# Performance work log

Measured on AMD Instinct MI355X. Metric: run time of the kernel, lower is better.

The kernel has to match this reference:

```python
import jax, jax.numpy as jnp
import numpy as np

EPS = 1e-7  # tf.keras.backend.epsilon()
ROUTINGS = 3


def setup_inputs() -> dict:
    key = jax.random.key(0)
    k1, k2 = jax.random.split(key)
    x = jax.random.normal(k1, (64, 2048, 8), dtype=jnp.float32)
    W = jax.random.normal(k2, (32, 2048, 16, 8), dtype=jnp.float32) * 0.05
    return {"x": x, "W": W}


def _squash(s):
    # source squash: vectors / sqrt(sum(v^2) + eps)
    ssq = jnp.sum(s * s, axis=-1, keepdims=True)
    return s / jnp.sqrt(ssq + EPS)


def reference(x, W):
    # x: [B, N, I]; W: [J, N, D, I]
    # prediction vectors u_hat: [B, J, N, D]
    u_hat = jnp.einsum('bni,jndi->bjnd', x, W)
    b = jnp.zeros(u_hat.shape[:-1], dtype=u_hat.dtype)  # [B, J, N]
    v = None
    for i in range(ROUTINGS):
        c = jax.nn.softmax(b, axis=1)                       # coupling over output caps J
        s = jnp.einsum('bjnd,bjn->bjd', u_hat, c)           # weighted sum over input caps N
        v = _squash(s)                                      # [B, J, D]
        if i < ROUTINGS - 1:
            b = b + jnp.einsum('bjnd,bjd->bjn', u_hat, v)   # agreement update
    return v
```

## Files before the change

### kernel.cpp

```cpp
#include <hip/hip_runtime.h>


#define BB_ 64
#define NN_ 2048
#define II_ 8
#define JJ_ 32
#define DD_ 16
#define NCHUNKS 128
#define CHUNK 16
#define BG 16
#define NBG (BB_ / BG)
#define EPS_ 1e-7f

#define PARTIAL_FLOATS (NCHUNKS * BB_ * JJ_ * DD_)

template <int CTRL>
__device__ __forceinline__ float dpp_add(float v) {
  const int s = __builtin_amdgcn_update_dpp(
      0, __builtin_bit_cast(int, v), CTRL, 0xf, 0xf, true);
  return v + __builtin_bit_cast(float, s);
}
#define DPP_QP_XOR1 0xB1
#define DPP_QP_XOR2 0x4E
#define DPP_HALF_MIRROR 0x141
#define DPP_ROR8 0x128

template <int PHASE>
__global__ __launch_bounds__(256, 2) void caps_phase(
    const float* __restrict__ x, const float* __restrict__ W,
    const float* __restrict__ V, float* __restrict__ partial) {
  const int tid = threadIdx.x;
  const int j = tid >> 3;
  const int p = tid & 7;
  const int chunk = blockIdx.x & (NCHUNKS - 1);
  const int bg = blockIdx.x >> 7;
  const int b0 = bg * BG;
  const int n0 = chunk * CHUNK;

  __shared__ float lmat[BG][JJ_];
  __shared__ float cmat[BG][JJ_];

  float v0r[BG], v1r[BG];
  if (PHASE > 0) {
#pragma unroll
    for (int b = 0; b < BG; ++b) {
      const float2 vv =
          *(const float2*)&V[((size_t)(b0 + b) * JJ_ + j) * DD_ + 2 * p];
      v0r[b] = vv.x;
      v1r[b] = vv.y;
    }
  }

  float s0[BG], s1[BG];
#pragma unroll
  for (int b = 0; b < BG; ++b) {
    s0[b] = 0.f;
    s1[b] = 0.f;
  }

  const float* wp = W + (size_t)j * (NN_ * DD_ * II_) + (size_t)n0 * (DD_ * II_) +
                    (size_t)p * 16;
  float4 wc0 = ((const float4*)wp)[0];
  float4 wc1 = ((const float4*)wp)[1];
  float4 wc2 = ((const float4*)wp)[2];
  float4 wc3 = ((const float4*)wp)[3];

  for (int nl = 0; nl < CHUNK; ++nl) {
    const int n = n0 + nl;
    const int nn = (nl + 1 < CHUNK) ? nl + 1 : nl;
    const float4* np_ = (const float4*)(wp + (size_t)nn * (DD_ * II_));
    const float4 wn0 = np_[0], wn1 = np_[1], wn2 = np_[2], wn3 = np_[3];

    float u0[BG], u1[BG];
#pragma unroll
    for (int b = 0; b < BG; ++b) {
      const float4* __restrict__ xr =
          (const float4*)(x + ((size_t)(b0 + b) * NN_ + n) * II_);
      const float4 xa = xr[0];
      const float4 xb = xr[1];
      u0[b] = wc0.x * xa.x + wc0.y * xa.y + wc0.z * xa.z + wc0.w * xa.w +
              wc1.x * xb.x + wc1.y * xb.y + wc1.z * xb.z + wc1.w * xb.w;
      u1[b] = wc2.x * xa.x + wc2.y * xa.y + wc2.z * xa.z + wc2.w * xa.w +
              wc3.x * xb.x + wc3.y * xb.y + wc3.z * xb.z + wc3.w * xb.w;
    }

    if (PHASE == 0) {
#pragma unroll
      for (int b = 0; b < BG; ++b) {
        s0[b] += u0[b];
        s1[b] += u1[b];
      }
    } else {
#pragma unroll
      for (int b = 0; b < BG; ++b) {
        float lp = u0[b] * v0r[b] + u1[b] * v1r[b];
        lp = dpp_add<DPP_QP_XOR1>(lp);
        lp = dpp_add<DPP_QP_XOR2>(lp);
        lp = dpp_add<DPP_HALF_MIRROR>(lp);
        if (p == 0) lmat[b][j] = lp;
      }
      __syncthreads();
      {
        const int jj = tid & 31;
        const int bb = tid >> 5;
        float e0 = __expf(lmat[bb][jj]);
        float e1 = __expf(lmat[bb + 8][jj]);
        float m0 = e0, m1 = e1;
        m0 = dpp_add<DPP_QP_XOR1>(m0);
        m1 = dpp_add<DPP_QP_XOR1>(m1);
        m0 = dpp_add<DPP_QP_XOR2>(m0);
        m1 = dpp_add<DPP_QP_XOR2>(m1);
        m0 = dpp_add<DPP_HALF_MIRROR>(m0);
        m1 = dpp_add<DPP_HALF_MIRROR>(m1);
        m0 = dpp_add<DPP_ROR8>(m0);
        m1 = dpp_add<DPP_ROR8>(m1);
        m0 += __shfl_xor(m0, 16);
        m1 += __shfl_xor(m1, 16);
        cmat[bb][jj] = e0 * __builtin_amdgcn_rcpf(m0);
        cmat[bb + 8][jj] = e1 * __builtin_amdgcn_rcpf(m1);
      }
      __syncthreads();
#pragma unroll
      for (int b = 0; b < BG; ++b) {
        const float c = cmat[b][j];
        s0[b] += c * u0[b];
        s1[b] += c * u1[b];
      }
    }

    wc0 = wn0;
    wc1 = wn1;
    wc2 = wn2;
    wc3 = wn3;
  }

  const float scale = (PHASE == 0) ? (1.0f / 32.0f) : 1.0f;
#pragma unroll
  for (int b = 0; b < BG; ++b) {
    const size_t off =
        ((size_t)chunk * BB_ + (b0 + b)) * (JJ_ * DD_) + j * DD_ + 2 * p;
    *(float2*)&partial[off] = make_float2(s0[b] * scale, s1[b] * scale);
  }
}

template <int MODE>
__global__ __launch_bounds__(256) void caps_reduce(
    const float* __restrict__ partial, float* __restrict__ V,
    float* __restrict__ out) {
  const int t = blockIdx.x * 256 + threadIdx.x;
  float s = 0.f;
#pragma unroll 8
  for (int c = 0; c < NCHUNKS; ++c)
    s += partial[(size_t)c * (BB_ * JJ_ * DD_) + t];
  float ss = s * s;
  ss += __shfl_xor(ss, 1);
  ss += __shfl_xor(ss, 2);
  ss += __shfl_xor(ss, 4);
  ss += __shfl_xor(ss, 8);
  const float v = s / sqrtf(ss + EPS_);
  if (MODE == 0)
    V[t] = v;
  else if (MODE == 1)
    V[t] += v;
  else
    out[t] = v;
}

extern "C" void kernel_launch(void* const* d_in, const int* in_sizes, int n_in,
                              void* d_out, int out_size, void* d_ws,
                              size_t ws_size, hipStream_t stream) {
  const float* x = (const float*)d_in[0];
  const float* W = (const float*)d_in[1];
  float* out = (float*)d_out;
  float* partial = (float*)d_ws;
  float* V = partial + PARTIAL_FLOATS;

  const dim3 kgrid(NBG * NCHUNKS);
  const dim3 rgrid((BB_ * JJ_ * DD_) / 256);

  caps_phase<0><<<kgrid, 256, 0, stream>>>(x, W, nullptr, partial);
  caps_reduce<0><<<rgrid, 256, 0, stream>>>(partial, V, out);
  caps_phase<1><<<kgrid, 256, 0, stream>>>(x, W, V, partial);
  caps_reduce<1><<<rgrid, 256, 0, stream>>>(partial, V, out);
  caps_phase<2><<<kgrid, 256, 0, stream>>>(x, W, V, partial);
  caps_reduce<2><<<rgrid, 256, 0, stream>>>(partial, V, out);
}
```

Baseline: 214.0 us.

## Halve batch group, raise occupancy, and use packed float2 FMAs

Cuts the per-block batch group from 16 to 8, which doubles the block count and raises the launch-bound occupancy target from 2 to 4 blocks per CU. The prediction dot products become float2 vector math, so the compiler can emit packed FP32 FMAs. The per-iteration softmax now handles one row per thread instead of two. The reduce kernels switch to 128-thread blocks. In exchange, each W chunk is read by twice as many blocks, which increases W traffic unless the cache absorbs it.

```diff
diff --git a/kernel.cpp b/kernel.cpp
--- a/kernel.cpp
+++ b/kernel.cpp
@@ -8,11 +8,13 @@
 #define DD_ 16
 #define NCHUNKS 128
 #define CHUNK 16
-#define BG 16
+#define BG 8
 #define NBG (BB_ / BG)
 #define EPS_ 1e-7f
 
 #define PARTIAL_FLOATS (NCHUNKS * BB_ * JJ_ * DD_)
+
+typedef __attribute__((ext_vector_type(2))) float v2f;
 
 template <int CTRL>
 __device__ __forceinline__ float dpp_add(float v) {
@@ -26,7 +28,7 @@
 #define DPP_ROR8 0x128
 
 template <int PHASE>
-__global__ __launch_bounds__(256, 2) void caps_phase(
+__global__ __launch_bounds__(256, 4) void caps_phase(
     const float* __restrict__ x, const float* __restrict__ W,
     const float* __restrict__ V, float* __restrict__ partial) {
   const int tid = threadIdx.x;
@@ -51,12 +53,9 @@
     }
   }
 
-  float s0[BG], s1[BG];
+  v2f s[BG];
 #pragma unroll
-  for (int b = 0; b < BG; ++b) {
-    s0[b] = 0.f;
-    s1[b] = 0.f;
-  }
+  for (int b = 0; b < BG; ++b) s[b] = (v2f)(0.f);
 
   const float* wp = W + (size_t)j * (NN_ * DD_ * II_) + (size_t)n0 * (DD_ * II_) +
                     (size_t)p * 16;
@@ -71,29 +70,36 @@
     const float4* np_ = (const float4*)(wp + (size_t)nn * (DD_ * II_));
     const float4 wn0 = np_[0], wn1 = np_[1], wn2 = np_[2], wn3 = np_[3];
 
-    float u0[BG], u1[BG];
+    v2f wk0 = {wc0.x, wc2.x}, wk1 = {wc0.y, wc2.y};
+    v2f wk2 = {wc0.z, wc2.z}, wk3 = {wc0.w, wc2.w};
+    v2f wk4 = {wc1.x, wc3.x}, wk5 = {wc1.y, wc3.y};
+    v2f wk6 = {wc1.z, wc3.z}, wk7 = {wc1.w, wc3.w};
+
+    v2f u[BG];
 #pragma unroll
     for (int b = 0; b < BG; ++b) {
       const float4* __restrict__ xr =
           (const float4*)(x + ((size_t)(b0 + b) * NN_ + n) * II_);
       const float4 xa = xr[0];
       const float4 xb = xr[1];
-      u0[b] = wc0.x * xa.x + wc0.y * xa.y + wc0.z * xa.z + wc0.w * xa.w +
-              wc1.x * xb.x + wc1.y * xb.y + wc1.z * xb.z + wc1.w * xb.w;
-      u1[b] = wc2.x * xa.x + wc2.y * xa.y + wc2.z * xa.z + wc2.w * xa.w +
-              wc3.x * xb.x + wc3.y * xb.y + wc3.z * xb.z + wc3.w * xb.w;
+      v2f acc = wk0 * xa.x;
+      acc += wk1 * xa.y;
+      acc += wk2 * xa.z;
+      acc += wk3 * xa.w;
+      acc += wk4 * xb.x;
+      acc += wk5 * xb.y;
+      acc += wk6 * xb.z;
+      acc += wk7 * xb.w;
+      u[b] = acc;
     }
 
     if (PHASE == 0) {
 #pragma unroll
-      for (int b = 0; b < BG; ++b) {
-        s0[b] += u0[b];
-        s1[b] += u1[b];
-      }
+      for (int b = 0; b < BG; ++b) s[b] += u[b];
     } else {
 #pragma unroll
       for (int b = 0; b < BG; ++b) {
-        float lp = u0[b] * v0r[b] + u1[b] * v1r[b];
+        float lp = u[b].x * v0r[b] + u[b].y * v1r[b];
         lp = dpp_add<DPP_QP_XOR1>(lp);
         lp = dpp_add<DPP_QP_XOR2>(lp);
         lp = dpp_add<DPP_HALF_MIRROR>(lp);
@@ -104,27 +110,19 @@
         const int jj = tid & 31;
         const int bb = tid >> 5;
         float e0 = __expf(lmat[bb][jj]);
-        float e1 = __expf(lmat[bb + 8][jj]);
-        float m0 = e0, m1 = e1;
+        float m0 = e0;
         m0 = dpp_add<DPP_QP_XOR1>(m0);
-        m1 = dpp_add<DPP_QP_XOR1>(m1);
         m0 = dpp_add<DPP_QP_XOR2>(m0);
-        m1 = dpp_add<DPP_QP_XOR2>(m1);
         m0 = dpp_add<DPP_HALF_MIRROR>(m0);
-        m1 = dpp_add<DPP_HALF_MIRROR>(m1);
         m0 = dpp_add<DPP_ROR8>(m0);
-        m1 = dpp_add<DPP_ROR8>(m1);
         m0 += __shfl_xor(m0, 16);
-        m1 += __shfl_xor(m1, 16);
         cmat[bb][jj] = e0 * __builtin_amdgcn_rcpf(m0);
-        cmat[bb + 8][jj] = e1 * __builtin_amdgcn_rcpf(m1);
       }
       __syncthreads();
 #pragma unroll
       for (int b = 0; b < BG; ++b) {
         const float c = cmat[b][j];
-        s0[b] += c * u0[b];
-        s1[b] += c * u1[b];
+        s[b] += u[b] * c;
       }
     }
 
@@ -139,15 +137,15 @@
   for (int b = 0; b < BG; ++b) {
     const size_t off =
         ((size_t)chunk * BB_ + (b0 + b)) * (JJ_ * DD_) + j * DD_ + 2 * p;
-    *(float2*)&partial[off] = make_float2(s0[b] * scale, s1[b] * scale);
+    *(float2*)&partial[off] = make_float2(s[b].x * scale, s[b].y * scale);
   }
 }
 
 template <int MODE>
-__global__ __launch_bounds__(256) void caps_reduce(
+__global__ __launch_bounds__(128) void caps_reduce(
     const float* __restrict__ partial, float* __restrict__ V,
     float* __restrict__ out) {
-  const int t = blockIdx.x * 256 + threadIdx.x;
+  const int t = blockIdx.x * 128 + threadIdx.x;
   float s = 0.f;
 #pragma unroll 8
   for (int c = 0; c < NCHUNKS; ++c)
@@ -176,12 +174,12 @@
   float* V = partial + PARTIAL_FLOATS;
 
   const dim3 kgrid(NBG * NCHUNKS);
-  const dim3 rgrid((BB_ * JJ_ * DD_) / 256);
+  const dim3 rgrid((BB_ * JJ_ * DD_) / 128);
 
   caps_phase<0><<<kgrid, 256, 0, stream>>>(x, W, nullptr, partial);
-  caps_reduce<0><<<rgrid, 256, 0, stream>>>(partial, V, out);
+  caps_reduce<0><<<rgrid, 128, 0, stream>>>(partial, V, out);
   caps_phase<1><<<kgrid, 256, 0, stream>>>(x, W, V, partial);
-  caps_reduce<1><<<rgrid, 256, 0, stream>>>(partial, V, out);
+  caps_reduce<1><<<rgrid, 128, 0, stream>>>(partial, V, out);
   caps_phase<2><<<kgrid, 256, 0, stream>>>(x, W, V, partial);
-  caps_reduce<2><<<rgrid, 256, 0, stream>>>(partial, V, out);
+  caps_reduce<2><<<rgrid, 128, 0, stream>>>(partial, V, out);
 }
```

New measurement: 177.9 us. 16.9% less time.
